# Optimization experiments

Measured on AMD Instinct MI355X. Metric: run time of the kernel, lower is better.

The kernel has to match this reference:

```python
import jax, jax.numpy as jnp
import numpy as np

B, C, H, W = 8, 256, 48, 48
CK = 64  # C // k
WSCALE = 0.3 / np.sqrt(C)  # keep exp(QK^T) finite (original has no 1/sqrt(d) scaling)


def conv1x1(x, w, b):
    # x: (B,C,H,W), w: (O,C,1,1), b: (O,) -> (B,O,H,W)
    return jnp.einsum('bchw,oc->bohw', x, w[:, :, 0, 0]) + b[None, :, None, None]


def setup_inputs() -> dict:
    key = jax.random.key(0)
    ks = jax.random.split(key, 6)
    x = jax.random.normal(ks[0], (B, C, H, W), dtype=jnp.float32)
    qw = jax.random.normal(ks[1], (CK, C, 1, 1), dtype=jnp.float32) * WSCALE
    kw = jax.random.normal(ks[2], (CK, C, 1, 1), dtype=jnp.float32) * WSCALE
    vw = jax.random.normal(ks[3], (C, C, 1, 1), dtype=jnp.float32) * (1.0 / np.sqrt(C))
    gw = jax.random.normal(ks[4], (C, C, 1, 1), dtype=jnp.float32) * (1.0 / np.sqrt(C))
    zk = jnp.zeros((CK,), dtype=jnp.float32)
    zc = jnp.zeros((C,), dtype=jnp.float32)
    return {
        'x': x,
        'query_weight': qw, 'query_bias': zk,
        'key_weight': kw, 'key_bias': zk,
        'value_weight': vw, 'value_bias': zc,
        'gamma_weight': gw, 'gamma_bias': zc,
        'k': 4,
    }


def reference(x, query_weight, query_bias, key_weight, key_bias,
              value_weight, value_bias, gamma_weight, gamma_bias, k):
    b, c, h, w = x.shape
    n = h * w
    q = conv1x1(x, query_weight, query_bias).reshape(b, -1, n)   # (B,Ck,N)
    kk = conv1x1(x, key_weight, key_bias).reshape(b, -1, n)      # (B,Ck,N)
    # energy[b,i,j] = q_i . k_j  (queries on rows, no sqrt(d) scaling)
    energy = jnp.einsum('bci,bcj->bij', q, kk)                   # (B,N,N)
    energy = jnp.exp(energy)
    energy = energy / jnp.sum(energy, axis=2, keepdims=True)     # unnormalized-softmax over keys
    v = conv1x1(x, value_weight, value_bias).reshape(b, c, n)    # (B,C,N)
    # out[b,c,j] = sum_i v[b,c,i] * energy[b,i,j]  (faithful to torch.bmm(V, energy))
    out = jnp.einsum('bci,bij->bcj', v, energy).reshape(b, c, h, w)
    out = conv1x1(out, gamma_weight, gamma_bias)
    return out
```

## Files before the change

### kernel.cpp

```cpp
#include <hip/hip_runtime.h>

#define BATCH 8
#define CIN   256
#define NPIX  2304
#define CKD   64
#define NIT   (NPIX / 16)
#define NIC   (NPIX / 32)
#define NJB   (NPIX / 64)

typedef _Float16 f16;
typedef __attribute__((ext_vector_type(4))) _Float16 f16x4;
typedef __attribute__((ext_vector_type(8))) _Float16 f16x8;
typedef __attribute__((ext_vector_type(4))) float    f32x4;


__global__ __launch_bounds__(256) void cast_w(
    const float* __restrict__ qw, const float* __restrict__ kw,
    f16* __restrict__ Wqk)
{
    int idx = (blockIdx.x * 256 + threadIdx.x) * 4;
    const float* src = (idx < 16384) ? qw + idx : kw + (idx - 16384);
    float4 v = *(const float4*)src;
    f16x4 h = { (f16)v.x, (f16)v.y, (f16)v.z, (f16)v.w };
    *(f16x4*)&Wqk[idx] = h;
}

__global__ __launch_bounds__(256) void make_wgv(
    const float* __restrict__ gw, const float* __restrict__ vw,
    const float* __restrict__ vb,
    f16* __restrict__ Wgv, float* __restrict__ b2)
{
    const int o = blockIdx.x, c2 = threadIdx.x;
    float s = 0.f;
    for (int c = 0; c < CIN; ++c)
        s += gw[o * CIN + c] * vw[(size_t)c * CIN + c2];
    Wgv[(size_t)o * CIN + c2] = (f16)s;
    if (c2 == 0) {
        float sb = 0.f;
        for (int c = 0; c < CIN; ++c) sb += gw[o * CIN + c] * vb[c];
        b2[o] = sb;
    }
}

__global__ __launch_bounds__(256) void cast_xT(
    const float* __restrict__ x, f16* __restrict__ xT)
{
    __shared__ float s[64][65];
    const int t = threadIdx.x;
    const int n0 = blockIdx.x * 64, c0 = blockIdx.y * 64, b = blockIdx.z;
    const float* xb = x + ((size_t)b * CIN + c0) * NPIX + n0;

    const int cl = t >> 4, ng = (t & 15) * 4;
    #pragma unroll
    for (int p = 0; p < 4; ++p) {
        float4 v = *(const float4*)(xb + (size_t)(cl + 16 * p) * NPIX + ng);
        s[cl + 16 * p][ng + 0] = v.x;
        s[cl + 16 * p][ng + 1] = v.y;
        s[cl + 16 * p][ng + 2] = v.z;
        s[cl + 16 * p][ng + 3] = v.w;
    }
    __syncthreads();
    const int nl = t >> 2, cs = (t & 3) * 16;
    f16 h[16];
    #pragma unroll
    for (int j = 0; j < 16; ++j) h[j] = (f16)s[cs + j][nl];
    f16* gp = &xT[((size_t)b * NPIX + n0 + nl) * CIN + c0 + cs];
    *(f16x8*)gp       = *(f16x8*)&h[0];
    *(f16x8*)(gp + 8) = *(f16x8*)&h[8];
}

__global__ __launch_bounds__(256) void qk_conv_mfma(
    const f16* __restrict__ xT, const f16* __restrict__ Wqk,
    const float* __restrict__ qbias, const float* __restrict__ kbias,
    f16* __restrict__ q_blk, f16* __restrict__ k_blk)
{
    __shared__ __align__(16) f16 us[32 * 136];
    const int t = threadIdx.x, w = t >> 6, lane = t & 63;
    const int quad = lane >> 4, l16 = lane & 15;
    const int wm = w & 1, wn = w >> 1;
    const int n0 = blockIdx.x * 32, b = blockIdx.y;

    const f16* bp = xT + ((size_t)b * NPIX + n0 + 16 * wn + l16) * CIN;
    const f16* ap = Wqk + (size_t)(64 * wm + l16) * CIN;

    f32x4 acc[4];
    #pragma unroll
    for (int mt = 0; mt < 4; ++mt) acc[mt] = (f32x4){0.f, 0.f, 0.f, 0.f};

    #pragma unroll
    for (int kk = 0; kk < CIN; kk += 32) {
        f16x8 bf = *(const f16x8*)(bp + kk + quad * 8);
        #pragma unroll
        for (int mt = 0; mt < 4; ++mt) {
            f16x8 af = *(const f16x8*)(ap + (size_t)mt * 16 * CIN + kk + quad * 8);
            acc[mt] = __builtin_amdgcn_mfma_f32_16x16x32_f16(af, bf, acc[mt], 0, 0, 0);
        }
    }
    const float* bias = wm ? kbias - 64 : qbias;
    #pragma unroll
    for (int mt = 0; mt < 4; ++mt) {
        int ob = 64 * wm + 16 * mt + quad * 4;
        #pragma unroll
        for (int r = 0; r < 4; ++r)
            us[(16 * wn + l16) * 136 + ob + r] = (f16)(acc[mt][r] + bias[ob + r]);
    }
    __syncthreads();
    {
        int ks2 = t >> 7, nt = (t >> 6) & 1, ln = t & 63;
        const f16* usr = &us[(nt * 16 + (ln & 15)) * 136 + ks2 * 32 + (ln >> 4) * 8];
        size_t base = (((size_t)b * NIT + (n0 >> 4) + nt) * 2 + ks2) * 512 + ln * 8;
        *(f16x8*)&q_blk[base] = *(const f16x8*)(usr);
        *(f16x8*)&k_blk[base] = *(const f16x8*)(usr + 64);
    }
}

#define ESL 136
__global__ __launch_bounds__(256) void energy_S(
    const f16* __restrict__ q_blk, const f16* __restrict__ k_blk,
    float* __restrict__ Pred)
{
    __shared__ __align__(16) f16 es[64 * ESL];
    __shared__ float red2[2][128];
    const int t    = threadIdx.x;
    const int w    = t >> 6, lane = t & 63;
    const int quad = lane >> 4, l16 = lane & 15;
    const int j0 = blockIdx.x * 64, i0 = blockIdx.y * 128, b = blockIdx.z;
    const size_t ln8 = (size_t)lane * 8;
    const f16* qb = q_blk + (size_t)b * NIT * 2 * 512 + ln8;

    f32x4 acc[8];
    #pragma unroll
    for (int mt = 0; mt < 8; ++mt) acc[mt] = (f32x4){0.f, 0.f, 0.f, 0.f};

    #pragma unroll
    for (int ks = 0; ks < 2; ++ks) {
        f16x8 bf = *(const f16x8*)(k_blk +
            (((size_t)b * NIT + (j0 >> 4) + w) * 2 + ks) * 512 + ln8);
        #pragma unroll
        for (int mt = 0; mt < 8; ++mt) {
            f16x8 af = *(const f16x8*)(qb + ((size_t)((i0 >> 4) + mt) * 2 + ks) * 512);
            acc[mt] = __builtin_amdgcn_mfma_f32_16x16x32_f16(af, bf, acc[mt], 0, 0, 0);
        }
    }

    #pragma unroll
    for (int mt = 0; mt < 8; ++mt) {
        f16x4 h = { (f16)__expf(acc[mt][0]), (f16)__expf(acc[mt][1]),
                    (f16)__expf(acc[mt][2]), (f16)__expf(acc[mt][3]) };
        *(f16x4*)&es[(16 * w + l16) * ESL + 16 * mt + quad * 4] = h;
    }
    __syncthreads();
    {
        int i = t & 127, jq = t >> 7;
        float s = 0.f;
        #pragma unroll
        for (int jj = 0; jj < 32; ++jj)
            s += (float)es[(jq * 32 + jj) * ESL + i];
        red2[jq][i] = s;
    }
    __syncthreads();
    if (t < 128)
        Pred[((size_t)blockIdx.x * BATCH + b) * NPIX + i0 + t] =
            red2[0][t] + red2[1][t];
}

__global__ __launch_bounds__(256) void reduce_S(
    const float* __restrict__ Pred, float* __restrict__ S)
{
    const size_t BN = (size_t)BATCH * NPIX;
    size_t idx = (size_t)blockIdx.x * 256 + threadIdx.x;
    float s = 0.f;
    #pragma unroll
    for (int jb = 0; jb < NJB; ++jb)
        s += Pred[(size_t)jb * BN + idx];
    S[idx] = s;
}

__global__ __launch_bounds__(256) void v_conv_mfma(
    const f16* __restrict__ xT, const f16* __restrict__ Wv,
    const float* __restrict__ vbias, const float* __restrict__ S,
    f16* __restrict__ u_blk)
{
    __shared__ __align__(16) f16 smem[9216];
    f16* As = smem;
    f16* Bs = smem + 128 * 40;
    f16* us = smem;
    const int t = threadIdx.x, w = t >> 6, lane = t & 63;
    const int quad = lane >> 4, l16 = lane & 15;
    const int wm = w & 1, wn = w >> 1;
    const int i0 = blockIdx.x * 64, c0 = blockIdx.y * 128, b = blockIdx.z;
    const int sub = t >> 2, le = t & 3;
    const f16* srcA = Wv + (size_t)(c0 + sub) * CIN + le * 8;
    const f16* srcB = xT + ((size_t)b * NPIX + i0 + sub) * CIN + le * 8;
    const int ldsw = sub * 40 + le * 8;

    f32x4 acc[4][2];
    #pragma unroll
    for (int mt = 0; mt < 4; ++mt)
        #pragma unroll
        for (int nt = 0; nt < 2; ++nt)
            acc[mt][nt] = (f32x4){0.f, 0.f, 0.f, 0.f};

    for (int kk = 0; kk < CIN; kk += 32) {
        f16x8 ta0 = *(const f16x8*)(srcA + kk);
        f16x8 ta1 = *(const f16x8*)(srcA + (size_t)64 * CIN + kk);
        f16x8 tb0 = *(const f16x8*)(srcB + kk);
        __syncthreads();
        *(f16x8*)&As[ldsw]           = ta0;
        *(f16x8*)&As[64 * 40 + ldsw] = ta1;
        *(f16x8*)&Bs[ldsw]           = tb0;
        __syncthreads();
        f16x8 af[4], bf[2];
        #pragma unroll
        for (int mt = 0; mt < 4; ++mt)
            af[mt] = *(const f16x8*)&As[(64 * wm + 16 * mt + l16) * 40 + quad * 8];
        #pragma unroll
        for (int nt = 0; nt < 2; ++nt)
            bf[nt] = *(const f16x8*)&Bs[(32 * wn + 16 * nt + l16) * 40 + quad * 8];
        #pragma unroll
        for (int mt = 0; mt < 4; ++mt)
            #pragma unroll
            for (int nt = 0; nt < 2; ++nt)
                acc[mt][nt] = __builtin_amdgcn_mfma_f32_16x16x32_f16(
                    af[mt], bf[nt], acc[mt][nt], 0, 0, 0);
    }

    __syncthreads();
    #pragma unroll
    for (int nt = 0; nt < 2; ++nt) {
        int i = 32 * wn + 16 * nt + l16;
        float is = 1.0f / S[(size_t)b * NPIX + i0 + i];
        #pragma unroll
        for (int mt = 0; mt < 4; ++mt)
            #pragma unroll
            for (int r = 0; r < 4; ++r) {
                int c = 64 * wm + 16 * mt + quad * 4 + r;
                us[c * 72 + i] = (f16)((acc[mt][nt][r] + vbias[c0 + c]) * is);
            }
    }
    __syncthreads();
    #pragma unroll
    for (int p = 0; p < 4; ++p) {
        int g  = t + 256 * p;
        int ct = g >> 7, ic = (g >> 6) & 1, ln = g & 63;
        f16x8 v = *(const f16x8*)&us[(ct * 16 + (ln & 15)) * 72 + ic * 32 + (ln >> 4) * 8];
        *(f16x8*)&u_blk[(((size_t)b * 16 + (c0 >> 4) + ct) * NIC + (i0 >> 5) + ic) * 512 + ln * 8] = v;
    }
}

__global__ __launch_bounds__(512, 4) void fused_bmm(
    const f16* __restrict__ q_blk, const f16* __restrict__ k_blk,
    const f16* __restrict__ u_blk, const float* __restrict__ gbias,
    float* __restrict__ out)
{
    extern __shared__ __align__(16) f16 es[];
    const int t = threadIdx.x, w = t >> 6, lane = t & 63;
    const int quad = lane >> 4, l16 = lane & 15;
    const int bid = blockIdx.x;
    const int b   = bid & 7;
    const int jb  = bid >> 3;
    const int j0  = jb * 64;
    const size_t ln8 = (size_t)lane * 8;

    const f16* qb = q_blk + (size_t)b * NIT * 2 * 512 + ln8;
    const f16* ub = u_blk + (size_t)b * 16 * NIC * 512 + ln8;

    const int iw0 = w >> 1;
    const int jh  = w & 1;

    f16x8 kf[2][2];
    #pragma unroll
    for (int jj = 0; jj < 2; ++jj)
        #pragma unroll
        for (int ks = 0; ks < 2; ++ks)
            kf[jj][ks] = *(const f16x8*)(k_blk +
                (((size_t)b * NIT + (j0 >> 4) + jh + 2 * jj) * 2 + ks) * 512 + ln8);

    const int CT0 = w * 2;
    const int woff = (quad >> 1) * 128 + l16 * 8 + (quad & 1) * 4;

    f32x4 acc[2][4];
    #pragma unroll
    for (int mt = 0; mt < 2; ++mt)
        #pragma unroll
        for (int jt = 0; jt < 4; ++jt)
            acc[mt][jt] = (f32x4){0.f, 0.f, 0.f, 0.f};

#define ULD(ct, icg) (*(const f16x8*)(ub + ((size_t)(CT0 + (ct)) * NIC + (icg)) * 512))

    #pragma unroll 1
    for (int gen = 0; gen < 8; ++gen) {
        const int t0 = gen * 18;
        for (int il = iw0; il < 18; il += 4) {
            const int gi = t0 + il;
            f16x8 q0 = *(const f16x8*)(qb + ((size_t)gi * 2 + 0) * 512);
            f16x8 q1 = *(const f16x8*)(qb + ((size_t)gi * 2 + 1) * 512);
            f32x4 e0 = (f32x4){0.f, 0.f, 0.f, 0.f};
            f32x4 e1 = (f32x4){0.f, 0.f, 0.f, 0.f};
            e0 = __builtin_amdgcn_mfma_f32_16x16x32_f16(q0, kf[0][0], e0, 0, 0, 0);
            e0 = __builtin_amdgcn_mfma_f32_16x16x32_f16(q1, kf[0][1], e0, 0, 0, 0);
            e1 = __builtin_amdgcn_mfma_f32_16x16x32_f16(q0, kf[1][0], e1, 0, 0, 0);
            e1 = __builtin_amdgcn_mfma_f32_16x16x32_f16(q1, kf[1][1], e1, 0, 0, 0);
            f16x4 h0 = { (f16)__expf(e0[0]), (f16)__expf(e0[1]),
                         (f16)__expf(e0[2]), (f16)__expf(e0[3]) };
            f16x4 h1 = { (f16)__expf(e1[0]), (f16)__expf(e1[1]),
                         (f16)__expf(e1[2]), (f16)__expf(e1[3]) };
            const int wo2 = ((il & 1) * 2) * 128 + woff;
            const int tb  = (il >> 1) * 4;
            *(f16x4*)&es[(size_t)(tb + jh) * 512 + wo2]     = h0;
            *(f16x4*)&es[(size_t)(tb + jh + 2) * 512 + wo2] = h1;
        }

        const int g0 = gen * 9;
        f16x8 ua = ULD(0, g0),     ub2 = ULD(1, g0);
        f16x8 na = ULD(0, g0 + 1), nb  = ULD(1, g0 + 1);
        asm volatile("s_waitcnt lgkmcnt(0)" ::: "memory");
        __builtin_amdgcn_s_barrier();

        __builtin_amdgcn_s_setprio(1);
        for (int ic2 = 0; ic2 < 9; ++ic2) {
            f16x8 fa, fb2;
            if (ic2 + 2 < 9) { fa = ULD(0, g0 + ic2 + 2); fb2 = ULD(1, g0 + ic2 + 2); }
            #pragma unroll
            for (int jt = 0; jt < 4; ++jt) {
                f16x8 bf = *(const f16x8*)&es[(size_t)(ic2 * 4 + jt) * 512 + ln8];
                acc[0][jt] = __builtin_amdgcn_mfma_f32_16x16x32_f16(ua,  bf, acc[0][jt], 0, 0, 0);
                acc[1][jt] = __builtin_amdgcn_mfma_f32_16x16x32_f16(ub2, bf, acc[1][jt], 0, 0, 0);
            }
            ua = na; ub2 = nb; na = fa; nb = fb2;
        }
        __builtin_amdgcn_s_setprio(0);
        __builtin_amdgcn_s_barrier();
    }
#undef ULD

    #pragma unroll
    for (int mt = 0; mt < 2; ++mt) {
        int cb = 32 * w + 16 * mt + quad * 4;
        #pragma unroll
        for (int jt = 0; jt < 4; ++jt) {
            int j = j0 + 16 * jt + l16;
            #pragma unroll
            for (int r = 0; r < 4; ++r)
                out[((size_t)b * CIN + cb + r) * NPIX + j] =
                    acc[mt][jt][r] + gbias[cb + r];
        }
    }
}

extern "C" void kernel_launch(void* const* d_in, const int* in_sizes, int n_in,
                              void* d_out, int out_size, void* d_ws, size_t ws_size,
                              hipStream_t stream) {
    const float* x   = (const float*)d_in[0];
    const float* qw  = (const float*)d_in[1];
    const float* qbv = (const float*)d_in[2];
    const float* kw  = (const float*)d_in[3];
    const float* kbv = (const float*)d_in[4];
    const float* vw  = (const float*)d_in[5];
    const float* vbv = (const float*)d_in[6];
    const float* gw  = (const float*)d_in[7];
    const float* gbv = (const float*)d_in[8];
    float* out = (float*)d_out;

    const size_t BCN  = (size_t)BATCH * CIN * NPIX;
    const size_t BN   = (size_t)BATCH * NPIX;
    const size_t BNCK = (size_t)BATCH * NPIX * CKD;

    f16* q_blk = (f16*)d_ws;
    f16* k_blk = q_blk + BNCK;
    f16* u_blk = k_blk + BNCK;
    f16* xT    = u_blk + BCN;
    f16* Wqk   = xT + BCN;
    f16* Wgv   = Wqk + 128 * 256;
    float* S   = (float*)(Wgv + 256 * 256);
    float* b2  = S + BN;
    float* Pred= b2 + 256;

    cast_w<<<32, 256, 0, stream>>>(qw, kw, Wqk);
    make_wgv<<<256, 256, 0, stream>>>(gw, vw, vbv, Wgv, b2);
    cast_xT<<<dim3(NPIX / 64, CIN / 64, BATCH), 256, 0, stream>>>(x, xT);
    qk_conv_mfma<<<dim3(NPIX / 32, BATCH), 256, 0, stream>>>(xT, Wqk, qbv, kbv, q_blk, k_blk);
    energy_S<<<dim3(NPIX / 64, NPIX / 128, BATCH), 256, 0, stream>>>(q_blk, k_blk, Pred);
    reduce_S<<<(int)(BN / 256), 256, 0, stream>>>(Pred, S);
    v_conv_mfma<<<dim3(NPIX / 64, CIN / 128, BATCH), 256, 0, stream>>>(xT, Wgv, b2, S, u_blk);
    fused_bmm<<<NJB * BATCH, 512, 36 * 1024, stream>>>(q_blk, k_blk, u_blk, gbv, out);
}
```

Baseline: 198.1 us.

## Use 1024-thread blocks in fused_bmm with finer per-wave work split

Doubles fused_bmm from 8 to 16 waves per block. Each wave now computes one 16-wide j tile of the exp(QK) energy tile instead of two, and in the V·E product handles 2 channel tiles by 2 j tiles instead of 2 by 4. The i-chunk per generation drops from 288 to 256 (9 generations of 16 tiles), so the shared tile shrinks to 32KB. This raises per-block parallelism and latency hiding and lowers per-wave register use, at the cost of more barrier participants and possibly fewer resident blocks per CU.

```diff
diff --git a/kernel.cpp b/kernel.cpp
--- a/kernel.cpp
+++ b/kernel.cpp
@@ -248,7 +248,7 @@
     }
 }
 
-__global__ __launch_bounds__(512, 4) void fused_bmm(
+__global__ __launch_bounds__(1024, 4) void fused_bmm(
     const f16* __restrict__ q_blk, const f16* __restrict__ k_blk,
     const f16* __restrict__ u_blk, const float* __restrict__ gbias,
     float* __restrict__ out)
@@ -265,69 +265,65 @@
     const f16* qb = q_blk + (size_t)b * NIT * 2 * 512 + ln8;
     const f16* ub = u_blk + (size_t)b * 16 * NIC * 512 + ln8;
 
-    const int iw0 = w >> 1;
-    const int jh  = w & 1;
-
-    f16x8 kf[2][2];
-    #pragma unroll
-    for (int jj = 0; jj < 2; ++jj)
-        #pragma unroll
-        for (int ks = 0; ks < 2; ++ks)
-            kf[jj][ks] = *(const f16x8*)(k_blk +
-                (((size_t)b * NIT + (j0 >> 4) + jh + 2 * jj) * 2 + ks) * 512 + ln8);
-
-    const int CT0 = w * 2;
+    const int jh = w & 3;
+    const int iw = w >> 2;
+    const int cg = w >> 1;
+    const int jg = w & 1;
+    const int CT0 = cg * 2;
+
+    f16x8 kf[2];
+    #pragma unroll
+    for (int ks = 0; ks < 2; ++ks)
+        kf[ks] = *(const f16x8*)(k_blk +
+            (((size_t)b * NIT + (j0 >> 4) + jh) * 2 + ks) * 512 + ln8);
+
     const int woff = (quad >> 1) * 128 + l16 * 8 + (quad & 1) * 4;
 
-    f32x4 acc[2][4];
+    f32x4 acc[2][2];
     #pragma unroll
     for (int mt = 0; mt < 2; ++mt)
         #pragma unroll
-        for (int jt = 0; jt < 4; ++jt)
+        for (int jt = 0; jt < 2; ++jt)
             acc[mt][jt] = (f32x4){0.f, 0.f, 0.f, 0.f};
 
 #define ULD(ct, icg) (*(const f16x8*)(ub + ((size_t)(CT0 + (ct)) * NIC + (icg)) * 512))
 
     #pragma unroll 1
-    for (int gen = 0; gen < 8; ++gen) {
-        const int t0 = gen * 18;
-        for (int il = iw0; il < 18; il += 4) {
+    for (int gen = 0; gen < 9; ++gen) {
+        const int t0 = gen * 16;
+        #pragma unroll
+        for (int s = 0; s < 4; ++s) {
+            const int il = iw + 4 * s;
             const int gi = t0 + il;
             f16x8 q0 = *(const f16x8*)(qb + ((size_t)gi * 2 + 0) * 512);
             f16x8 q1 = *(const f16x8*)(qb + ((size_t)gi * 2 + 1) * 512);
             f32x4 e0 = (f32x4){0.f, 0.f, 0.f, 0.f};
-            f32x4 e1 = (f32x4){0.f, 0.f, 0.f, 0.f};
-            e0 = __builtin_amdgcn_mfma_f32_16x16x32_f16(q0, kf[0][0], e0, 0, 0, 0);
-            e0 = __builtin_amdgcn_mfma_f32_16x16x32_f16(q1, kf[0][1], e0, 0, 0, 0);
-            e1 = __builtin_amdgcn_mfma_f32_16x16x32_f16(q0, kf[1][0], e1, 0, 0, 0);
-            e1 = __builtin_amdgcn_mfma_f32_16x16x32_f16(q1, kf[1][1], e1, 0, 0, 0);
+            e0 = __builtin_amdgcn_mfma_f32_16x16x32_f16(q0, kf[0], e0, 0, 0, 0);
+            e0 = __builtin_amdgcn_mfma_f32_16x16x32_f16(q1, kf[1], e0, 0, 0, 0);
             f16x4 h0 = { (f16)__expf(e0[0]), (f16)__expf(e0[1]),
                          (f16)__expf(e0[2]), (f16)__expf(e0[3]) };
-            f16x4 h1 = { (f16)__expf(e1[0]), (f16)__expf(e1[1]),
-                         (f16)__expf(e1[2]), (f16)__expf(e1[3]) };
             const int wo2 = ((il & 1) * 2) * 128 + woff;
             const int tb  = (il >> 1) * 4;
-            *(f16x4*)&es[(size_t)(tb + jh) * 512 + wo2]     = h0;
-            *(f16x4*)&es[(size_t)(tb + jh + 2) * 512 + wo2] = h1;
-        }
-
-        const int g0 = gen * 9;
-        f16x8 ua = ULD(0, g0),     ub2 = ULD(1, g0);
-        f16x8 na = ULD(0, g0 + 1), nb  = ULD(1, g0 + 1);
+            *(f16x4*)&es[(size_t)(tb + jh) * 512 + wo2] = h0;
+        }
+
+        const int g0 = gen * 8;
+        f16x8 ua0 = ULD(0, g0),     ua1 = ULD(1, g0);
+        f16x8 na0 = ULD(0, g0 + 1), na1 = ULD(1, g0 + 1);
         asm volatile("s_waitcnt lgkmcnt(0)" ::: "memory");
         __builtin_amdgcn_s_barrier();
 
         __builtin_amdgcn_s_setprio(1);
-        for (int ic2 = 0; ic2 < 9; ++ic2) {
-            f16x8 fa, fb2;
-            if (ic2 + 2 < 9) { fa = ULD(0, g0 + ic2 + 2); fb2 = ULD(1, g0 + ic2 + 2); }
-            #pragma unroll
-            for (int jt = 0; jt < 4; ++jt) {
-                f16x8 bf = *(const f16x8*)&es[(size_t)(ic2 * 4 + jt) * 512 + ln8];
-                acc[0][jt] = __builtin_amdgcn_mfma_f32_16x16x32_f16(ua,  bf, acc[0][jt], 0, 0, 0);
-                acc[1][jt] = __builtin_amdgcn_mfma_f32_16x16x32_f16(ub2, bf, acc[1][jt], 0, 0, 0);
-            }
-            ua = na; ub2 = nb; na = fa; nb = fb2;
+        for (int ic2 = 0; ic2 < 8; ++ic2) {
+            f16x8 fa0, fa1;
+            if (ic2 + 2 < 8) { fa0 = ULD(0, g0 + ic2 + 2); fa1 = ULD(1, g0 + ic2 + 2); }
+            f16x8 bf0 = *(const f16x8*)&es[(size_t)(ic2 * 4 + jg * 2 + 0) * 512 + ln8];
+            f16x8 bf1 = *(const f16x8*)&es[(size_t)(ic2 * 4 + jg * 2 + 1) * 512 + ln8];
+            acc[0][0] = __builtin_amdgcn_mfma_f32_16x16x32_f16(ua0, bf0, acc[0][0], 0, 0, 0);
+            acc[1][0] = __builtin_amdgcn_mfma_f32_16x16x32_f16(ua1, bf0, acc[1][0], 0, 0, 0);
+            acc[0][1] = __builtin_amdgcn_mfma_f32_16x16x32_f16(ua0, bf1, acc[0][1], 0, 0, 0);
+            acc[1][1] = __builtin_amdgcn_mfma_f32_16x16x32_f16(ua1, bf1, acc[1][1], 0, 0, 0);
+            ua0 = na0; ua1 = na1; na0 = fa0; na1 = fa1;
         }
         __builtin_amdgcn_s_setprio(0);
         __builtin_amdgcn_s_barrier();
@@ -336,10 +332,10 @@
 
     #pragma unroll
     for (int mt = 0; mt < 2; ++mt) {
-        int cb = 32 * w + 16 * mt + quad * 4;
-        #pragma unroll
-        for (int jt = 0; jt < 4; ++jt) {
-            int j = j0 + 16 * jt + l16;
+        int cb = (CT0 + mt) * 16 + quad * 4;
+        #pragma unroll
+        for (int jt = 0; jt < 2; ++jt) {
+            int j = j0 + (jg * 2 + jt) * 16 + l16;
             #pragma unroll
             for (int r = 0; r < 4; ++r)
                 out[((size_t)b * CIN + cb + r) * NPIX + j] =
@@ -383,5 +379,5 @@
     energy_S<<<dim3(NPIX / 64, NPIX / 128, BATCH), 256, 0, stream>>>(q_blk, k_blk, Pred);
     reduce_S<<<(int)(BN / 256), 256, 0, stream>>>(Pred, S);
     v_conv_mfma<<<dim3(NPIX / 64, CIN / 128, BATCH), 256, 0, stream>>>(xT, Wgv, b2, S, u_blk);
-    fused_bmm<<<NJB * BATCH, 512, 36 * 1024, stream>>>(q_blk, k_blk, u_blk, gbv, out);
-}
+    fused_bmm<<<NJB * BATCH, 1024, 32 * 1024, stream>>>(q_blk, k_blk, u_blk, gbv, out);
+}
```

New measurement: 226.6 us. 14.4% more time.
